# Kernel optimization log

Hardware: AMD Instinct MI355X
Metric: run time of the kernel (lower is better)

The kernel has to match this reference:

```python
import jax, jax.numpy as jnp
import numpy as np

B, S, T, D, H, DF, E = 16, 1024, 512, 512, 8, 2048, 4
DH = D // H
EPS = 1e-5


def setup_inputs() -> dict:
    key = jax.random.key(0)
    ks = iter(jax.random.split(key, 64))

    def nrm(shape, scale=0.02):
        return jax.random.normal(next(ks), shape, dtype=jnp.float32) * scale

    inp = {
        "x": jax.random.normal(next(ks), (B, S, D), dtype=jnp.float32),
        "cross": jax.random.normal(next(ks), (B, T, D), dtype=jnp.float32),
    }
    for p in ("sa", "ca"):
        for w in ("wq", "wk", "wv", "wo"):
            inp[f"{p}_{w}"] = nrm((D, D))
            inp[f"{p}_b{w[1]}"] = jnp.zeros((D,), jnp.float32)
    inp["gate_w"] = nrm((D, E))
    inp["gate_b"] = jnp.zeros((E,), jnp.float32)
    inp["exp_w1"] = nrm((E, D, DF))
    inp["exp_b1"] = jnp.zeros((E, DF), jnp.float32)
    inp["exp_w2"] = nrm((E, DF, D))
    inp["exp_b2"] = jnp.zeros((E, D), jnp.float32)
    for i in (1, 2, 3):
        inp[f"n{i}_g"] = jnp.ones((D,), jnp.float32)
        inp[f"n{i}_b"] = jnp.zeros((D,), jnp.float32)
    return inp


def layer_norm(x, g, b):
    m = x.mean(-1, keepdims=True)
    v = x.var(-1, keepdims=True)
    return (x - m) * jax.lax.rsqrt(v + EPS) * g + b


def mha(q_in, kv_in, wq, bq, wk, bk, wv, bv, wo, bo, causal):
    Bq, Sq, _ = q_in.shape
    Sk = kv_in.shape[1]
    q = (q_in @ wq + bq).reshape(Bq, Sq, H, DH)
    k = (kv_in @ wk + bk).reshape(Bq, Sk, H, DH)
    v = (kv_in @ wv + bv).reshape(Bq, Sk, H, DH)
    scores = jnp.einsum('bshd,bthd->bhst', q, k) / jnp.sqrt(jnp.float32(DH))
    if causal:
        mask = jnp.tril(jnp.ones((Sq, Sk), dtype=bool))
        scores = jnp.where(mask, scores, jnp.float32(-1e9))
    attn = jax.nn.softmax(scores, axis=-1)
    out = jnp.einsum('bhst,bthd->bshd', attn, v).reshape(Bq, Sq, D)
    return out @ wo + bo


def moe_ffn(x, gw, gb, w1, b1, w2, b2):
    gates = jax.nn.softmax(x @ gw + gb, axis=-1)            # [B,S,E]
    h = jax.nn.relu(jnp.einsum('bsd,edf->bsef', x, w1) + b1)  # [B,S,E,DF]
    yo = jnp.einsum('bsef,efd->bsed', h, w2) + b2            # [B,S,E,D]
    y = jnp.einsum('bse,bsed->bsd', gates, yo)
    imp = gates.mean((0, 1))                                 # importance per expert
    aux = jnp.float32(E) * jnp.sum(imp * imp)                # load-balance penalty
    return y, aux


def reference(x, cross,
              sa_wq, sa_bq, sa_wk, sa_bk, sa_wv, sa_bv, sa_wo, sa_bo,
              ca_wq, ca_bq, ca_wk, ca_bk, ca_wv, ca_bv, ca_wo, ca_bo,
              gate_w, gate_b, exp_w1, exp_b1, exp_w2, exp_b2,
              n1_g, n1_b, n2_g, n2_b, n3_g, n3_b):
    # dropout is identity in eval mode
    x = x + mha(x, x, sa_wq, sa_bq, sa_wk, sa_bk, sa_wv, sa_bv, sa_wo, sa_bo, causal=True)
    x = layer_norm(x, n1_g, n1_b)
    x = x + mha(x, cross, ca_wq, ca_bq, ca_wk, ca_bk, ca_wv, ca_bv, ca_wo, ca_bo, causal=False)
    x = layer_norm(x, n2_g, n2_b)
    y, aux_loss = moe_ffn(x, gate_w, gate_b, exp_w1, exp_b1, exp_w2, exp_b2)
    out = layer_norm(x + y, n3_g, n3_b)
    return out, aux_loss
```

## Files before the change

kernel.cpp:

```cpp
#include <hip/hip_runtime.h>
#include <stdint.h>
#include <stddef.h>

typedef unsigned short bf16u;
typedef __attribute__((ext_vector_type(8))) short short8;
typedef __attribute__((ext_vector_type(4))) float f32x4;

__device__ __forceinline__ bf16u f2bf(float f) {
  union { float f; unsigned u; } v; v.f = f;
  unsigned r = v.u + 0x7FFFu + ((v.u >> 16) & 1u);
  return (bf16u)(r >> 16);
}

#define GL16(g, l) __builtin_amdgcn_global_load_lds( \
    (const __attribute__((address_space(1))) unsigned int*)(g), \
    (__attribute__((address_space(3))) unsigned int*)(l), 16, 0, 0)

enum { EPI_BF16 = 0, EPI_BF16_RELU = 1, EPI_VT = 2, EPI_RES = 3, EPI_GATE = 4 };

template<int EPI>
__global__ __launch_bounds__(256, 2) void gemm_k(
    const bf16u* __restrict__ A, const bf16u* __restrict__ BT,
    const float* __restrict__ bias, const float* __restrict__ res,
    const float* __restrict__ gates,
    bf16u* __restrict__ outb, float* __restrict__ outf,
    int M, int N, int K, int slog, int egate, int firste)
{
  __shared__ bf16u Ab[2][128 * 32];
  __shared__ bf16u Bb[2][128 * 32];
  const int tid = threadIdx.x, lane = tid & 63, w = tid >> 6;
  const int wm = w >> 1, wn = w & 1;
  const int nbt = N >> 7;
  const int mt = blockIdx.x / nbt, nt = blockIdx.x - mt * nbt;
  const int bm = mt << 7, bn = nt << 7;

  const int srow = lane >> 2;
  const int scol = (lane & 3) << 3;
  const bf16u* ap0 = A + (size_t)(bm + w * 16 + srow) * K + scol;
  const bf16u* ap1 = ap0 + (size_t)64 * K;
  const bf16u* bp0 = BT + (size_t)(bn + w * 16 + srow) * K + scol;
  const bf16u* bp1 = bp0 + (size_t)64 * K;

  f32x4 acc[4][4] = {};
  const int NT = K >> 5;

  GL16(ap0, &Ab[0][w * 512]);
  GL16(ap1, &Ab[0][(4 + w) * 512]);
  GL16(bp0, &Bb[0][w * 512]);
  GL16(bp1, &Bb[0][(4 + w) * 512]);
  __syncthreads();

  const int rl = lane & 15, kg = (lane >> 4) << 3;
  int cur = 0;
  for (int kt = 0; kt < NT; ++kt) {
    if (kt + 1 < NT) {
      const int ko = (kt + 1) << 5;
      const int nb = cur ^ 1;
      GL16(ap0 + ko, &Ab[nb][w * 512]);
      GL16(ap1 + ko, &Ab[nb][(4 + w) * 512]);
      GL16(bp0 + ko, &Bb[nb][w * 512]);
      GL16(bp1 + ko, &Bb[nb][(4 + w) * 512]);
    }
    short8 af[4], bfv[4];
    #pragma unroll
    for (int i = 0; i < 4; ++i)
      af[i] = *(const short8*)&Ab[cur][(wm * 64 + i * 16 + rl) * 32 + kg];
    #pragma unroll
    for (int j = 0; j < 4; ++j)
      bfv[j] = *(const short8*)&Bb[cur][(wn * 64 + j * 16 + rl) * 32 + kg];
    #pragma unroll
    for (int i = 0; i < 4; ++i)
      #pragma unroll
      for (int j = 0; j < 4; ++j)
        acc[i][j] = __builtin_amdgcn_mfma_f32_16x16x32_bf16(af[i], bfv[j], acc[i][j], 0, 0, 0);
    __syncthreads();
    cur ^= 1;
  }

  const int r0 = bm + wm * 64, c0 = bn + wn * 64;
  const int rsub = (lane >> 4) << 2;
  #pragma unroll
  for (int j = 0; j < 4; ++j) {
    const int col = c0 + j * 16 + rl;
    const float bs = bias ? bias[col] : 0.f;
    #pragma unroll
    for (int i = 0; i < 4; ++i) {
      const f32x4 v = acc[i][j];
      #pragma unroll
      for (int jj = 0; jj < 4; ++jj) {
        const int row = r0 + i * 16 + rsub + jj;
        float val = v[jj] + bs;
        if (EPI == EPI_BF16) {
          outb[(size_t)row * N + col] = f2bf(val);
        } else if (EPI == EPI_BF16_RELU) {
          outb[(size_t)row * N + col] = f2bf(val > 0.f ? val : 0.f);
        } else if (EPI == EPI_VT) {
          const int b_ = row >> slog, t_ = row & ((1 << slog) - 1);
          outb[(((size_t)(b_ * 8 + (col >> 6)) << 6) + (size_t)(col & 63)) * ((size_t)1 << slog) + t_] = f2bf(val);
        } else if (EPI == EPI_RES) {
          outf[(size_t)row * N + col] = res[(size_t)row * N + col] + val;
        } else {
          const float g = gates[(size_t)row * 4 + egate];
          const size_t oi = (size_t)row * N + col;
          const float c = g * val;
          outf[oi] = firste ? c : (outf[oi] + c);
        }
      }
    }
  }
}

template<bool CAUSAL>
__global__ __launch_bounds__(256, 2) void attn_k(
    const bf16u* __restrict__ Q, const bf16u* __restrict__ Kg,
    const bf16u* __restrict__ VT, bf16u* __restrict__ O,
    int Sq, int Sk)
{
  __shared__ bf16u Kl[64 * 64];
  __shared__ bf16u Vl[64 * 64];
  __shared__ bf16u Pl[64 * 64];
  const int nqt = Sq >> 6;
  const int bh = blockIdx.x / nqt, qt = blockIdx.x - bh * nqt;
  const int b = bh >> 3, h = bh & 7;
  const int tid = threadIdx.x, lane = tid & 63, w = tid >> 6;
  const int rl = lane & 15, g4 = lane >> 4;

  const int qrow = qt * 64 + w * 16 + rl;
  const bf16u* qp = Q + (size_t)(b * Sq + qrow) * 512 + h * 64 + g4 * 8;
  const short8 qf0 = *(const short8*)qp;
  const short8 qf1 = *(const short8*)(qp + 32);

  f32x4 oacc[4] = {};
  float ml = -1e30f, ll = 0.f;
  const int KT = CAUSAL ? (qt + 1) : (Sk >> 6);

  const int str = tid >> 2, stc = tid & 3;
  const int sw_st = (str & 7) << 4;
  const bf16u* kq = Kg + (size_t)(b * Sk + str) * 512 + h * 64 + stc * 8;
  const bf16u* vq = VT + (size_t)(bh * 64 + str) * Sk + stc * 8;
  char* const klw0 = (char*)Kl + str * 128 + ((stc * 16) ^ sw_st);
  char* const klw1 = (char*)Kl + str * 128 + ((stc * 16 + 64) ^ sw_st);
  char* const vlw0 = (char*)Vl + str * 128 + ((stc * 16) ^ sw_st);
  char* const vlw1 = (char*)Vl + str * 128 + ((stc * 16 + 64) ^ sw_st);

  const int qr = w * 16 + rl;
  char* const pbase = (char*)Pl + qr * 128;
  const int swq = (qr & 7) << 4;

  for (int kt = 0; kt < KT; ++kt) {
    __syncthreads();
    {
      const bf16u* ks = kq + (size_t)kt * 64 * 512;
      const bf16u* vs = vq + kt * 64;
      *(short8*)klw0 = *(const short8*)ks;
      *(short8*)klw1 = *(const short8*)(ks + 32);
      *(short8*)vlw0 = *(const short8*)vs;
      *(short8*)vlw1 = *(const short8*)(vs + 32);
    }
    __syncthreads();

    f32x4 st[4] = {};
    #pragma unroll
    for (int mi = 0; mi < 4; ++mi) {
      const int kr = mi * 16 + rl;
      const char* kb_ = (const char*)Kl + kr * 128;
      const int sw = (kr & 7) << 4;
      const short8 kf0 = *(const short8*)(kb_ + ((g4 * 16) ^ sw));
      const short8 kf1 = *(const short8*)(kb_ + ((g4 * 16 + 64) ^ sw));
      st[mi] = __builtin_amdgcn_mfma_f32_16x16x32_bf16(kf0, qf0, st[mi], 0, 0, 0);
      st[mi] = __builtin_amdgcn_mfma_f32_16x16x32_bf16(kf1, qf1, st[mi], 0, 0, 0);
    }

    const int qg = qt * 64 + qr;
    float sv[16];
    float pm = -1e30f;
    #pragma unroll
    for (int mi = 0; mi < 4; ++mi) {
      #pragma unroll
      for (int jj = 0; jj < 4; ++jj) {
        float s = st[mi][jj] * 0.125f;
        if (CAUSAL) {
          const int kgi = kt * 64 + mi * 16 + g4 * 4 + jj;
          if (kgi > qg) s = -1e30f;
        }
        sv[mi * 4 + jj] = s;
        pm = fmaxf(pm, s);
      }
    }
    pm = fmaxf(pm, __shfl_xor(pm, 16));
    pm = fmaxf(pm, __shfl_xor(pm, 32));
    const float mnew = fmaxf(ml, pm);
    const float alpha = exp2f((ml - mnew) * 1.44269504f);
    float ps = 0.f;
    bf16u pb[16];
    #pragma unroll
    for (int ii = 0; ii < 16; ++ii) {
      const float p = exp2f((sv[ii] - mnew) * 1.44269504f);
      ps += p;
      pb[ii] = f2bf(p);
    }
    ps += __shfl_xor(ps, 16);
    ps += __shfl_xor(ps, 32);
    ll = ll * alpha + ps;
    ml = mnew;

    #pragma unroll
    for (int jj = 0; jj < 4; ++jj) {
      const float aj = __shfl(alpha, g4 * 4 + jj);
      #pragma unroll
      for (int ni = 0; ni < 4; ++ni) oacc[ni][jj] *= aj;
    }

    #pragma unroll
    for (int mi = 0; mi < 4; ++mi) {
      #pragma unroll
      for (int jp = 0; jp < 2; ++jp) {
        const unsigned pk = (unsigned)pb[mi * 4 + jp * 2] | ((unsigned)pb[mi * 4 + jp * 2 + 1] << 16);
        const int kx2 = mi * 32 + g4 * 8 + jp * 4;
        *(unsigned*)(pbase + (kx2 ^ swq)) = pk;
      }
    }
    asm volatile("s_waitcnt lgkmcnt(0)" ::: "memory");
    #pragma unroll
    for (int ks = 0; ks < 2; ++ks) {
      const short8 pf = *(const short8*)(pbase + ((g4 * 16 + ks * 64) ^ swq));
      #pragma unroll
      for (int ni = 0; ni < 4; ++ni) {
        const int vr = ni * 16 + rl;
        const short8 vf = *(const short8*)((const char*)Vl + vr * 128 + ((g4 * 16 + ks * 64) ^ ((vr & 7) << 4)));
        oacc[ni] = __builtin_amdgcn_mfma_f32_16x16x32_bf16(pf, vf, oacc[ni], 0, 0, 0);
      }
    }
  }

  #pragma unroll
  for (int jj = 0; jj < 4; ++jj) {
    const float lj = __shfl(ll, g4 * 4 + jj);
    const float inv = 1.f / lj;
    const int row = qt * 64 + w * 16 + g4 * 4 + jj;
    #pragma unroll
    for (int ni = 0; ni < 4; ++ni)
      O[(size_t)(b * Sq + row) * 512 + h * 64 + ni * 16 + rl] = f2bf(oacc[ni][jj] * inv);
  }
}

template<bool ADD, bool BOUT>
__global__ __launch_bounds__(256, 4) void ln_k(
    const float* __restrict__ X, const float* __restrict__ Y,
    const float* __restrict__ gam, const float* __restrict__ bet,
    float* __restrict__ outf, bf16u* __restrict__ outb)
{
  const int row = blockIdx.x * 4 + (threadIdx.x >> 6);
  const int lane = threadIdx.x & 63;
  const float* xp = X + (size_t)row * 512 + lane * 8;
  float v[8];
  {
    const float4 t0 = *(const float4*)xp;
    const float4 t1 = *(const float4*)(xp + 4);
    v[0] = t0.x; v[1] = t0.y; v[2] = t0.z; v[3] = t0.w;
    v[4] = t1.x; v[5] = t1.y; v[6] = t1.z; v[7] = t1.w;
  }
  if (ADD) {
    const float* yp = Y + (size_t)row * 512 + lane * 8;
    const float4 t0 = *(const float4*)yp;
    const float4 t1 = *(const float4*)(yp + 4);
    v[0] += t0.x; v[1] += t0.y; v[2] += t0.z; v[3] += t0.w;
    v[4] += t1.x; v[5] += t1.y; v[6] += t1.z; v[7] += t1.w;
  }
  float s = 0.f, q = 0.f;
  #pragma unroll
  for (int i = 0; i < 8; ++i) { s += v[i]; q += v[i] * v[i]; }
  #pragma unroll
  for (int off = 1; off < 64; off <<= 1) {
    s += __shfl_xor(s, off);
    q += __shfl_xor(q, off);
  }
  const float mean = s * (1.f / 512.f);
  const float var = q * (1.f / 512.f) - mean * mean;
  const float rs = rsqrtf(var + 1e-5f);
  float gv[8], bv[8];
  {
    const float4 t0 = *(const float4*)(gam + lane * 8);
    const float4 t1 = *(const float4*)(gam + lane * 8 + 4);
    gv[0] = t0.x; gv[1] = t0.y; gv[2] = t0.z; gv[3] = t0.w;
    gv[4] = t1.x; gv[5] = t1.y; gv[6] = t1.z; gv[7] = t1.w;
    const float4 u0 = *(const float4*)(bet + lane * 8);
    const float4 u1 = *(const float4*)(bet + lane * 8 + 4);
    bv[0] = u0.x; bv[1] = u0.y; bv[2] = u0.z; bv[3] = u0.w;
    bv[4] = u1.x; bv[5] = u1.y; bv[6] = u1.z; bv[7] = u1.w;
  }
  float o[8];
  #pragma unroll
  for (int i = 0; i < 8; ++i) o[i] = (v[i] - mean) * rs * gv[i] + bv[i];
  float* op = outf + (size_t)row * 512 + lane * 8;
  *(float4*)op = make_float4(o[0], o[1], o[2], o[3]);
  *(float4*)(op + 4) = make_float4(o[4], o[5], o[6], o[7]);
  if (BOUT) {
    union { bf16u u[8]; short8 v8; } pk;
    #pragma unroll
    for (int i = 0; i < 8; ++i) pk.u[i] = f2bf(o[i]);
    *(short8*)(outb + (size_t)row * 512 + lane * 8) = pk.v8;
  }
}

__global__ __launch_bounds__(256, 4) void gate_k(
    const float* __restrict__ X, const float* __restrict__ gw,
    const float* __restrict__ gb, float* __restrict__ gates,
    float* __restrict__ imp)
{
  __shared__ float sh[4];
  const int tid = threadIdx.x;
  if (tid < 4) sh[tid] = 0.f;
  __syncthreads();
  const int row = blockIdx.x * 4 + (tid >> 6);
  const int lane = tid & 63;
  const float* xr = X + (size_t)row * 512;
  float a0 = 0.f, a1 = 0.f, a2 = 0.f, a3 = 0.f;
  for (int d = lane; d < 512; d += 64) {
    const float xv = xr[d];
    const float4 wv = *(const float4*)(gw + d * 4);
    a0 += xv * wv.x; a1 += xv * wv.y; a2 += xv * wv.z; a3 += xv * wv.w;
  }
  #pragma unroll
  for (int off = 1; off < 64; off <<= 1) {
    a0 += __shfl_xor(a0, off); a1 += __shfl_xor(a1, off);
    a2 += __shfl_xor(a2, off); a3 += __shfl_xor(a3, off);
  }
  if (lane == 0) {
    a0 += gb[0]; a1 += gb[1]; a2 += gb[2]; a3 += gb[3];
    const float m = fmaxf(fmaxf(a0, a1), fmaxf(a2, a3));
    const float e0 = exp2f((a0 - m) * 1.44269504f);
    const float e1 = exp2f((a1 - m) * 1.44269504f);
    const float e2 = exp2f((a2 - m) * 1.44269504f);
    const float e3 = exp2f((a3 - m) * 1.44269504f);
    const float inv = 1.f / (e0 + e1 + e2 + e3);
    float* gr = gates + (size_t)row * 4;
    const float g0 = e0 * inv, g1 = e1 * inv, g2 = e2 * inv, g3 = e3 * inv;
    gr[0] = g0; gr[1] = g1; gr[2] = g2; gr[3] = g3;
    atomicAdd(&sh[0], g0); atomicAdd(&sh[1], g1);
    atomicAdd(&sh[2], g2); atomicAdd(&sh[3], g3);
  }
  __syncthreads();
  if (tid < 4) atomicAdd(&imp[tid], sh[tid]);
}

__global__ void aux_k(const float* __restrict__ imp, float* __restrict__ out) {
  if (threadIdx.x == 0 && blockIdx.x == 0) {
    float s = 0.f;
    #pragma unroll
    for (int e = 0; e < 4; ++e) { const float v = imp[e] * (1.f / 16384.f); s += v * v; }
    out[0] = 4.f * s;
  }
}

__global__ __launch_bounds__(256, 4) void conv_k(const float* __restrict__ in, bf16u* __restrict__ out) {
  const size_t i = ((size_t)blockIdx.x * 256 + threadIdx.x) * 8;
  const float4 a = *(const float4*)(in + i);
  const float4 b = *(const float4*)(in + i + 4);
  union { bf16u u[8]; short8 v; } pk;
  pk.u[0] = f2bf(a.x); pk.u[1] = f2bf(a.y); pk.u[2] = f2bf(a.z); pk.u[3] = f2bf(a.w);
  pk.u[4] = f2bf(b.x); pk.u[5] = f2bf(b.y); pk.u[6] = f2bf(b.z); pk.u[7] = f2bf(b.w);
  *(short8*)(out + i) = pk.v;
}

__global__ __launch_bounds__(256, 4) void trans_k(
    const float* __restrict__ W, bf16u* __restrict__ WT, int K, int N)
{
  __shared__ float t[32][33];
  const int tx = threadIdx.x & 31, ty = threadIdx.x >> 5;
  const int n0 = blockIdx.x * 32, k0 = blockIdx.y * 32;
  #pragma unroll
  for (int i = 0; i < 4; ++i)
    t[ty + i * 8][tx] = W[(size_t)(k0 + ty + i * 8) * N + n0 + tx];
  __syncthreads();
  #pragma unroll
  for (int i = 0; i < 4; ++i)
    WT[(size_t)(n0 + ty + i * 8) * K + k0 + tx] = f2bf(t[tx][ty + i * 8]);
}

extern "C" void kernel_launch(void* const* d_in, const int* in_sizes, int n_in,
                              void* d_out, int out_size, void* d_ws, size_t ws_size,
                              hipStream_t stream)
{
  const int B = 16, S = 1024, T = 512, D = 512, DF = 2048, E = 4;
  const int M = B * S;
  const int Mc = B * T;
  (void)in_sizes; (void)n_in; (void)out_size; (void)ws_size;

  const float* x      = (const float*)d_in[0];
  const float* cross  = (const float*)d_in[1];
  const float* gate_w = (const float*)d_in[18];
  const float* gate_b = (const float*)d_in[19];
  const float* exp_w1 = (const float*)d_in[20];
  const float* exp_b1 = (const float*)d_in[21];
  const float* exp_w2 = (const float*)d_in[22];
  const float* exp_b2 = (const float*)d_in[23];

  char* p = (char*)d_ws;
  auto alloc = [&](size_t bytes) -> char* {
    char* r = p;
    p += (bytes + 255) & ~(size_t)255;
    return r;
  };
  bf16u* xb    = (bf16u*)alloc((size_t)M * D * 2);
  bf16u* crb   = (bf16u*)alloc((size_t)Mc * D * 2);
  bf16u* wT    = (bf16u*)alloc((size_t)8 * D * D * 2);
  bf16u* w1T   = (bf16u*)alloc((size_t)E * DF * D * 2);
  bf16u* w2T   = (bf16u*)alloc((size_t)E * D * DF * 2);
  bf16u* qb    = (bf16u*)alloc((size_t)M * D * 2);
  bf16u* kb    = (bf16u*)alloc((size_t)M * D * 2);
  bf16u* vTb   = (bf16u*)alloc((size_t)M * D * 2);
  bf16u* ao    = (bf16u*)alloc((size_t)M * D * 2);
  float* xf    = (float*)alloc((size_t)M * D * 4);
  bf16u* x2b   = (bf16u*)alloc((size_t)M * D * 2);
  float* gates = (float*)alloc((size_t)M * 4 * 4);
  float* imp   = (float*)alloc(256);
  bf16u* hbuf  = (bf16u*)alloc((size_t)M * DF * 2);
  float* y     = (float*)alloc((size_t)M * D * 4);

  hipMemsetAsync(imp, 0, 32, stream);
  conv_k<<<(M * D) / 2048, 256, 0, stream>>>(x, xb);
  conv_k<<<(Mc * D) / 2048, 256, 0, stream>>>(cross, crb);
  for (int i = 0; i < 8; ++i)
    trans_k<<<dim3(D / 32, D / 32), 256, 0, stream>>>((const float*)d_in[2 + 2 * i], wT + (size_t)i * D * D, D, D);
  for (int e = 0; e < E; ++e)
    trans_k<<<dim3(DF / 32, D / 32), 256, 0, stream>>>(exp_w1 + (size_t)e * D * DF, w1T + (size_t)e * DF * D, D, DF);
  for (int e = 0; e < E; ++e)
    trans_k<<<dim3(D / 32, DF / 32), 256, 0, stream>>>(exp_w2 + (size_t)e * DF * D, w2T + (size_t)e * D * DF, DF, D);

  const int gMD  = (M / 128) * (D / 128);
  const int gMcD = (Mc / 128) * (D / 128);
  const int gMDF = (M / 128) * (DF / 128);

  gemm_k<EPI_BF16><<<gMD, 256, 0, stream>>>(xb, wT + 0 * (size_t)D * D, (const float*)d_in[3], nullptr, nullptr, qb, nullptr, M, D, D, 0, 0, 0);
  gemm_k<EPI_BF16><<<gMD, 256, 0, stream>>>(xb, wT + 1 * (size_t)D * D, (const float*)d_in[5], nullptr, nullptr, kb, nullptr, M, D, D, 0, 0, 0);
  gemm_k<EPI_VT><<<gMD, 256, 0, stream>>>(xb, wT + 2 * (size_t)D * D, (const float*)d_in[7], nullptr, nullptr, vTb, nullptr, M, D, D, 10, 0, 0);
  attn_k<true><<<B * 8 * (S / 64), 256, 0, stream>>>(qb, kb, vTb, ao, S, S);
  gemm_k<EPI_RES><<<gMD, 256, 0, stream>>>(ao, wT + 3 * (size_t)D * D, (const float*)d_in[9], x, nullptr, nullptr, xf, M, D, D, 0, 0, 0);
  ln_k<false, true><<<M / 4, 256, 0, stream>>>(xf, nullptr, (const float*)d_in[24], (const float*)d_in[25], xf, x2b);

  gemm_k<EPI_BF16><<<gMD, 256, 0, stream>>>(x2b, wT + 4 * (size_t)D * D, (const float*)d_in[11], nullptr, nullptr, qb, nullptr, M, D, D, 0, 0, 0);
  gemm_k<EPI_BF16><<<gMcD, 256, 0, stream>>>(crb, wT + 5 * (size_t)D * D, (const float*)d_in[13], nullptr, nullptr, kb, nullptr, Mc, D, D, 0, 0, 0);
  gemm_k<EPI_VT><<<gMcD, 256, 0, stream>>>(crb, wT + 6 * (size_t)D * D, (const float*)d_in[15], nullptr, nullptr, vTb, nullptr, Mc, D, D, 9, 0, 0);
  attn_k<false><<<B * 8 * (S / 64), 256, 0, stream>>>(qb, kb, vTb, ao, S, T);
  gemm_k<EPI_RES><<<gMD, 256, 0, stream>>>(ao, wT + 7 * (size_t)D * D, (const float*)d_in[17], xf, nullptr, nullptr, xf, M, D, D, 0, 0, 0);
  ln_k<false, true><<<M / 4, 256, 0, stream>>>(xf, nullptr, (const float*)d_in[26], (const float*)d_in[27], xf, x2b);

  gate_k<<<M / 4, 256, 0, stream>>>(xf, gate_w, gate_b, gates, imp);
  aux_k<<<1, 64, 0, stream>>>(imp, (float*)d_out + (size_t)M * D);
  for (int e = 0; e < E; ++e) {
    gemm_k<EPI_BF16_RELU><<<gMDF, 256, 0, stream>>>(x2b, w1T + (size_t)e * DF * D, exp_b1 + (size_t)e * DF, nullptr, nullptr, hbuf, nullptr, M, DF, D, 0, 0, 0);
    gemm_k<EPI_GATE><<<gMD, 256, 0, stream>>>(hbuf, w2T + (size_t)e * D * DF, exp_b2 + (size_t)e * D, nullptr, gates, nullptr, y, M, D, DF, 0, e, e == 0 ? 1 : 0);
  }
  ln_k<true, false><<<M / 4, 256, 0, stream>>>(xf, y, (const float*)d_in[28], (const float*)d_in[29], (float*)d_out, nullptr);
}
```

Measured before the change: 1.001 ms.

## Double-buffer attention K/V tiles and move MoE gate scaling into first GEMM

The attention kernel now prefetches the next K/V tile into registers while the current tile is computed, using two LDS buffers so one barrier pair per iteration can be avoided. The softmax scale is folded into the log2 constant, and the causal mask is applied only on the diagonal tile. In the MoE, the gate is applied to the relu output of the first GEMM and the second GEMM only accumulates. The gated expert bias b2 is added in a new final layernorm kernel. Risks include higher register and LDS use with the occupancy hint raised to 4, and bf16 rounding of gated activations.

```diff
diff --git a/kernel.cpp b/kernel.cpp
--- a/kernel.cpp
+++ b/kernel.cpp
@@ -16,7 +16,7 @@
     (const __attribute__((address_space(1))) unsigned int*)(g), \
     (__attribute__((address_space(3))) unsigned int*)(l), 16, 0, 0)
 
-enum { EPI_BF16 = 0, EPI_BF16_RELU = 1, EPI_VT = 2, EPI_RES = 3, EPI_GATE = 4 };
+enum { EPI_BF16 = 0, EPI_RELU_GATE = 1, EPI_VT = 2, EPI_RES = 3, EPI_ACC = 4 };
 
 template<int EPI>
 __global__ __launch_bounds__(256, 2) void gemm_k(
@@ -92,18 +92,17 @@
         float val = v[jj] + bs;
         if (EPI == EPI_BF16) {
           outb[(size_t)row * N + col] = f2bf(val);
-        } else if (EPI == EPI_BF16_RELU) {
-          outb[(size_t)row * N + col] = f2bf(val > 0.f ? val : 0.f);
+        } else if (EPI == EPI_RELU_GATE) {
+          const float g = gates[(size_t)row * 4 + egate];
+          outb[(size_t)row * N + col] = f2bf(g * (val > 0.f ? val : 0.f));
         } else if (EPI == EPI_VT) {
           const int b_ = row >> slog, t_ = row & ((1 << slog) - 1);
           outb[(((size_t)(b_ * 8 + (col >> 6)) << 6) + (size_t)(col & 63)) * ((size_t)1 << slog) + t_] = f2bf(val);
         } else if (EPI == EPI_RES) {
           outf[(size_t)row * N + col] = res[(size_t)row * N + col] + val;
         } else {
-          const float g = gates[(size_t)row * 4 + egate];
           const size_t oi = (size_t)row * N + col;
-          const float c = g * val;
-          outf[oi] = firste ? c : (outf[oi] + c);
+          outf[oi] = firste ? val : (outf[oi] + val);
         }
       }
     }
@@ -111,13 +110,13 @@
 }
 
 template<bool CAUSAL>
-__global__ __launch_bounds__(256, 2) void attn_k(
+__global__ __launch_bounds__(256, 4) void attn_k(
     const bf16u* __restrict__ Q, const bf16u* __restrict__ Kg,
     const bf16u* __restrict__ VT, bf16u* __restrict__ O,
     int Sq, int Sk)
 {
-  __shared__ bf16u Kl[64 * 64];
-  __shared__ bf16u Vl[64 * 64];
+  __shared__ bf16u Kl[2][64 * 64];
+  __shared__ bf16u Vl[2][64 * 64];
   __shared__ bf16u Pl[64 * 64];
   const int nqt = Sq >> 6;
   const int bh = blockIdx.x / nqt, qt = blockIdx.x - bh * nqt;
@@ -138,32 +137,45 @@
   const int sw_st = (str & 7) << 4;
   const bf16u* kq = Kg + (size_t)(b * Sk + str) * 512 + h * 64 + stc * 8;
   const bf16u* vq = VT + (size_t)(bh * 64 + str) * Sk + stc * 8;
-  char* const klw0 = (char*)Kl + str * 128 + ((stc * 16) ^ sw_st);
-  char* const klw1 = (char*)Kl + str * 128 + ((stc * 16 + 64) ^ sw_st);
-  char* const vlw0 = (char*)Vl + str * 128 + ((stc * 16) ^ sw_st);
-  char* const vlw1 = (char*)Vl + str * 128 + ((stc * 16 + 64) ^ sw_st);
+  const int lo0 = str * 128 + ((stc * 16) ^ sw_st);
+  const int lo1 = str * 128 + ((stc * 16 + 64) ^ sw_st);
 
   const int qr = w * 16 + rl;
   char* const pbase = (char*)Pl + qr * 128;
   const int swq = (qr & 7) << 4;
 
+  {
+    const short8 k0 = *(const short8*)kq;
+    const short8 k1 = *(const short8*)(kq + 32);
+    const short8 v0 = *(const short8*)vq;
+    const short8 v1 = *(const short8*)(vq + 32);
+    *(short8*)((char*)Kl[0] + lo0) = k0;
+    *(short8*)((char*)Kl[0] + lo1) = k1;
+    *(short8*)((char*)Vl[0] + lo0) = v0;
+    *(short8*)((char*)Vl[0] + lo1) = v1;
+  }
+  __syncthreads();
+
+  int cur = 0;
   for (int kt = 0; kt < KT; ++kt) {
-    __syncthreads();
-    {
-      const bf16u* ks = kq + (size_t)kt * 64 * 512;
-      const bf16u* vs = vq + kt * 64;
-      *(short8*)klw0 = *(const short8*)ks;
-      *(short8*)klw1 = *(const short8*)(ks + 32);
-      *(short8*)vlw0 = *(const short8*)vs;
-      *(short8*)vlw1 = *(const short8*)(vs + 32);
-    }
-    __syncthreads();
-
+    short8 nk0, nk1, nv0, nv1;
+    const bool pre = (kt + 1 < KT);
+    if (pre) {
+      const bf16u* ks = kq + (size_t)(kt + 1) * 64 * 512;
+      const bf16u* vs = vq + (kt + 1) * 64;
+      nk0 = *(const short8*)ks;
+      nk1 = *(const short8*)(ks + 32);
+      nv0 = *(const short8*)vs;
+      nv1 = *(const short8*)(vs + 32);
+    }
+
+    const bf16u* Kc = Kl[cur];
+    const bf16u* Vc = Vl[cur];
     f32x4 st[4] = {};
     #pragma unroll
     for (int mi = 0; mi < 4; ++mi) {
       const int kr = mi * 16 + rl;
-      const char* kb_ = (const char*)Kl + kr * 128;
+      const char* kb_ = (const char*)Kc + kr * 128;
       const int sw = (kr & 7) << 4;
       const short8 kf0 = *(const short8*)(kb_ + ((g4 * 16) ^ sw));
       const short8 kf1 = *(const short8*)(kb_ + ((g4 * 16 + 64) ^ sw));
@@ -171,31 +183,40 @@
       st[mi] = __builtin_amdgcn_mfma_f32_16x16x32_bf16(kf1, qf1, st[mi], 0, 0, 0);
     }
 
-    const int qg = qt * 64 + qr;
+    const float SC = 0.125f * 1.44269504f;
     float sv[16];
     float pm = -1e30f;
-    #pragma unroll
-    for (int mi = 0; mi < 4; ++mi) {
-      #pragma unroll
-      for (int jj = 0; jj < 4; ++jj) {
-        float s = st[mi][jj] * 0.125f;
-        if (CAUSAL) {
+    if (CAUSAL && kt == qt) {
+      const int qg = qt * 64 + qr;
+      #pragma unroll
+      for (int mi = 0; mi < 4; ++mi)
+        #pragma unroll
+        for (int jj = 0; jj < 4; ++jj) {
+          float s = st[mi][jj] * SC;
           const int kgi = kt * 64 + mi * 16 + g4 * 4 + jj;
           if (kgi > qg) s = -1e30f;
+          sv[mi * 4 + jj] = s;
+          pm = fmaxf(pm, s);
         }
-        sv[mi * 4 + jj] = s;
-        pm = fmaxf(pm, s);
-      }
+    } else {
+      #pragma unroll
+      for (int mi = 0; mi < 4; ++mi)
+        #pragma unroll
+        for (int jj = 0; jj < 4; ++jj) {
+          const float s = st[mi][jj] * SC;
+          sv[mi * 4 + jj] = s;
+          pm = fmaxf(pm, s);
+        }
     }
     pm = fmaxf(pm, __shfl_xor(pm, 16));
     pm = fmaxf(pm, __shfl_xor(pm, 32));
     const float mnew = fmaxf(ml, pm);
-    const float alpha = exp2f((ml - mnew) * 1.44269504f);
+    const float alpha = exp2f(ml - mnew);
     float ps = 0.f;
     bf16u pb[16];
     #pragma unroll
     for (int ii = 0; ii < 16; ++ii) {
-      const float p = exp2f((sv[ii] - mnew) * 1.44269504f);
+      const float p = exp2f(sv[ii] - mnew);
       ps += p;
       pb[ii] = f2bf(p);
     }
@@ -227,10 +248,21 @@
       #pragma unroll
       for (int ni = 0; ni < 4; ++ni) {
         const int vr = ni * 16 + rl;
-        const short8 vf = *(const short8*)((const char*)Vl + vr * 128 + ((g4 * 16 + ks * 64) ^ ((vr & 7) << 4)));
+        const short8 vf = *(const short8*)((const char*)Vc + vr * 128 + ((g4 * 16 + ks * 64) ^ ((vr & 7) << 4)));
         oacc[ni] = __builtin_amdgcn_mfma_f32_16x16x32_bf16(pf, vf, oacc[ni], 0, 0, 0);
       }
     }
+
+    __syncthreads();
+    if (pre) {
+      const int nb = cur ^ 1;
+      *(short8*)((char*)Kl[nb] + lo0) = nk0;
+      *(short8*)((char*)Kl[nb] + lo1) = nk1;
+      *(short8*)((char*)Vl[nb] + lo0) = nv0;
+      *(short8*)((char*)Vl[nb] + lo1) = nv1;
+      __syncthreads();
+    }
+    cur ^= 1;
   }
 
   #pragma unroll
@@ -278,20 +310,12 @@
   const float mean = s * (1.f / 512.f);
   const float var = q * (1.f / 512.f) - mean * mean;
   const float rs = rsqrtf(var + 1e-5f);
-  float gv[8], bv[8];
-  {
-    const float4 t0 = *(const float4*)(gam + lane * 8);
-    const float4 t1 = *(const float4*)(gam + lane * 8 + 4);
-    gv[0] = t0.x; gv[1] = t0.y; gv[2] = t0.z; gv[3] = t0.w;
-    gv[4] = t1.x; gv[5] = t1.y; gv[6] = t1.z; gv[7] = t1.w;
-    const float4 u0 = *(const float4*)(bet + lane * 8);
-    const float4 u1 = *(const float4*)(bet + lane * 8 + 4);
-    bv[0] = u0.x; bv[1] = u0.y; bv[2] = u0.z; bv[3] = u0.w;
-    bv[4] = u1.x; bv[5] = u1.y; bv[6] = u1.z; bv[7] = u1.w;
-  }
   float o[8];
   #pragma unroll
-  for (int i = 0; i < 8; ++i) o[i] = (v[i] - mean) * rs * gv[i] + bv[i];
+  for (int i = 0; i < 8; ++i) {
+    const float g = gam[lane * 8 + i], bb = bet[lane * 8 + i];
+    o[i] = (v[i] - mean) * rs * g + bb;
+  }
   float* op = outf + (size_t)row * 512 + lane * 8;
   *(float4*)op = make_float4(o[0], o[1], o[2], o[3]);
   *(float4*)(op + 4) = make_float4(o[4], o[5], o[6], o[7]);
@@ -301,6 +325,54 @@
     for (int i = 0; i < 8; ++i) pk.u[i] = f2bf(o[i]);
     *(short8*)(outb + (size_t)row * 512 + lane * 8) = pk.v8;
   }
+}
+
+__global__ __launch_bounds__(256, 4) void ln_final_k(
+    const float* __restrict__ X, const float* __restrict__ Y,
+    const float* __restrict__ gates, const float* __restrict__ b2,
+    const float* __restrict__ gam, const float* __restrict__ bet,
+    float* __restrict__ outf)
+{
+  const int row = blockIdx.x * 4 + (threadIdx.x >> 6);
+  const int lane = threadIdx.x & 63;
+  const float4 gv4 = *(const float4*)(gates + (size_t)row * 4);
+  float v[8];
+  {
+    const float* xp = X + (size_t)row * 512 + lane * 8;
+    const float* yp = Y + (size_t)row * 512 + lane * 8;
+    const float4 t0 = *(const float4*)xp;
+    const float4 t1 = *(const float4*)(xp + 4);
+    const float4 u0 = *(const float4*)yp;
+    const float4 u1 = *(const float4*)(yp + 4);
+    v[0] = t0.x + u0.x; v[1] = t0.y + u0.y; v[2] = t0.z + u0.z; v[3] = t0.w + u0.w;
+    v[4] = t1.x + u1.x; v[5] = t1.y + u1.y; v[6] = t1.z + u1.z; v[7] = t1.w + u1.w;
+  }
+  #pragma unroll
+  for (int e = 0; e < 4; ++e) {
+    const float ge = e == 0 ? gv4.x : e == 1 ? gv4.y : e == 2 ? gv4.z : gv4.w;
+    const float4 b0 = *(const float4*)(b2 + e * 512 + lane * 8);
+    const float4 b1 = *(const float4*)(b2 + e * 512 + lane * 8 + 4);
+    v[0] += ge * b0.x; v[1] += ge * b0.y; v[2] += ge * b0.z; v[3] += ge * b0.w;
+    v[4] += ge * b1.x; v[5] += ge * b1.y; v[6] += ge * b1.z; v[7] += ge * b1.w;
+  }
+  float s = 0.f, q = 0.f;
+  #pragma unroll
+  for (int i = 0; i < 8; ++i) { s += v[i]; q += v[i] * v[i]; }
+  #pragma unroll
+  for (int off = 1; off < 64; off <<= 1) {
+    s += __shfl_xor(s, off);
+    q += __shfl_xor(q, off);
+  }
+  const float mean = s * (1.f / 512.f);
+  const float var = q * (1.f / 512.f) - mean * mean;
+  const float rs = rsqrtf(var + 1e-5f);
+  float* op = outf + (size_t)row * 512 + lane * 8;
+  float o[8];
+  #pragma unroll
+  for (int i = 0; i < 8; ++i)
+    o[i] = (v[i] - mean) * rs * gam[lane * 8 + i] + bet[lane * 8 + i];
+  *(float4*)op = make_float4(o[0], o[1], o[2], o[3]);
+  *(float4*)(op + 4) = make_float4(o[4], o[5], o[6], o[7]);
 }
 
 __global__ __launch_bounds__(256, 4) void gate_k(
@@ -449,8 +521,8 @@
   gate_k<<<M / 4, 256, 0, stream>>>(xf, gate_w, gate_b, gates, imp);
   aux_k<<<1, 64, 0, stream>>>(imp, (float*)d_out + (size_t)M * D);
   for (int e = 0; e < E; ++e) {
-    gemm_k<EPI_BF16_RELU><<<gMDF, 256, 0, stream>>>(x2b, w1T + (size_t)e * DF * D, exp_b1 + (size_t)e * DF, nullptr, nullptr, hbuf, nullptr, M, DF, D, 0, 0, 0);
-    gemm_k<EPI_GATE><<<gMD, 256, 0, stream>>>(hbuf, w2T + (size_t)e * D * DF, exp_b2 + (size_t)e * D, nullptr, gates, nullptr, y, M, D, DF, 0, e, e == 0 ? 1 : 0);
-  }
-  ln_k<true, false><<<M / 4, 256, 0, stream>>>(xf, y, (const float*)d_in[28], (const float*)d_in[29], (float*)d_out, nullptr);
-}
+    gemm_k<EPI_RELU_GATE><<<gMDF, 256, 0, stream>>>(x2b, w1T + (size_t)e * DF * D, exp_b1 + (size_t)e * DF, nullptr, gates, hbuf, nullptr, M, DF, D, 0, e, 0);
+    gemm_k<EPI_ACC><<<gMD, 256, 0, stream>>>(hbuf, w2T + (size_t)e * D * DF, nullptr, nullptr, nullptr, nullptr, y, M, D, DF, 0, 0, e == 0 ? 1 : 0);
+  }
+  ln_final_k<<<M / 4, 256, 0, stream>>>(xf, y, gates, exp_b2, (const float*)d_in[28], (const float*)d_in[29], (float*)d_out);
+}
```

New measurement: 1.010 ms. About the same (+0.9%).
